# Performance work log

Hardware: AMD Instinct MI355X
Metric: run time of the kernel (lower is better)

The kernel has to match this reference:

```python
import jax, jax.numpy as jnp
import numpy as np

N_ATOMS = 100_000
N_PAIRS = 6_400_000
CUTOFF = 5.0
CUTON = 4.0


def setup_inputs() -> dict:
    key = jax.random.key(0)
    k = jax.random.split(key, 4)
    atomic_numbers = jax.random.uniform(k[0], (N_ATOMS,), jnp.float32, 1.0, 94.0)
    displacements = jax.random.normal(k[1], (N_PAIRS, 3), jnp.float32) * 2.0
    idx_i = jnp.sort(jax.random.randint(k[2], (N_PAIRS,), 0, N_ATOMS, jnp.int32))
    idx_j = jax.random.randint(k[3], (N_PAIRS,), 0, N_ATOMS, jnp.int32)
    atom_mask = jnp.ones((N_ATOMS,), jnp.float32)
    batch_segments = jnp.zeros((N_ATOMS,), jnp.int32)
    batch_mask = jnp.ones((N_PAIRS,), jnp.float32)
    # ZBL parameters (non-trainable constants from setup())
    a_coefficient = jnp.asarray(0.8854, jnp.float32)
    a_exponent = jnp.asarray(0.23, jnp.float32)
    phi_coefficients = jnp.array([0.18175, 0.50986, 0.28022, 0.02817], jnp.float32)
    phi_exponents = jnp.array([3.1998, 0.94229, 0.4029, 0.20162], jnp.float32)
    return dict(
        atomic_numbers=atomic_numbers,
        displacements=displacements,
        idx_i=idx_i,
        idx_j=idx_j,
        atom_mask=atom_mask,
        batch_segments=batch_segments,
        batch_mask=batch_mask,
        batch_size=1,
        a_coefficient=a_coefficient,
        a_exponent=a_exponent,
        phi_coefficients=phi_coefficients,
        phi_exponents=phi_exponents,
    )


def _switch_fn(distances):
    # smooth 1 -> 0 switch between CUTON and CUTOFF
    x = (CUTOFF - distances) / (CUTOFF - CUTON)
    poly = ((6.0 * x - 15.0) * x + 10.0) * x ** 3
    return jnp.where(distances < CUTON, 1.0, jnp.where(distances >= CUTOFF, 0.0, poly))


def reference(atomic_numbers, displacements, idx_i, idx_j, atom_mask,
              batch_segments, batch_mask, batch_size,
              a_coefficient, a_exponent, phi_coefficients, phi_exponents):
    distances = jnp.maximum(jnp.linalg.norm(displacements, axis=-1), 1e-10)  # [E]
    switch_off = _switch_fn(distances)

    za = jnp.power(atomic_numbers, jnp.abs(a_exponent))  # [N]
    denominator = jnp.maximum(za[idx_i] + za[idx_j], 1e-10)  # [E]
    a_ij = jnp.abs(a_coefficient) / denominator
    arguments = distances / a_ij  # [E]

    coefficients = jax.nn.softmax(jnp.abs(phi_coefficients))  # [4]
    exponents = jnp.abs(phi_exponents)  # [4]
    log_terms = -exponents[None, :] * arguments[:, None]  # [E,4]
    max_log = jnp.max(log_terms, axis=1, keepdims=True)
    # NOTE: faithful to the original -- max_log is never added back
    phi = jnp.sum(coefficients[None, :] * jnp.exp(log_terms - max_log), axis=1)  # [E]

    log_repulsion = (jnp.log(0.5)
                     + jnp.log(atomic_numbers[idx_i])
                     + jnp.log(atomic_numbers[idx_j])
                     - jnp.log(distances)
                     + jnp.log(jnp.maximum(phi, 1e-30))
                     + jnp.log(jnp.maximum(switch_off, 1e-30)))
    repulsion = jnp.exp(log_repulsion) * batch_mask  # [E]

    Erep = jax.ops.segment_sum(repulsion, segment_ids=idx_i,
                               num_segments=atomic_numbers.shape[0])  # [N]
    Erep = Erep * atom_mask
    return Erep[..., None, None, None]
```

## Files before the change

kernel.cpp:

```cpp
#include <hip/hip_runtime.h>
#include <math.h>


__global__ __launch_bounds__(256) void zbl_prep_kernel(
    const float* __restrict__ z, const float* __restrict__ a_coef,
    const float* __restrict__ a_exp, const float* __restrict__ phi_c,
    const float* __restrict__ phi_e, float2* __restrict__ tab,
    float* __restrict__ out, float* __restrict__ consts, int n_atoms) {
  int n = blockIdx.x * blockDim.x + threadIdx.x;
  if (n < n_atoms) {
    float zi = z[n];
    float ae = fabsf(a_exp[0]);
    tab[n] = make_float2(zi, powf(zi, ae));
    out[n] = 0.0f;
  }
  if (blockIdx.x == 0 && threadIdx.x == 0) {
    float c[4];
    float m = -1e30f;
    for (int k = 0; k < 4; ++k) { c[k] = fabsf(phi_c[k]); m = fmaxf(m, c[k]); }
    float s = 0.0f;
    for (int k = 0; k < 4; ++k) { c[k] = expf(c[k] - m); s += c[k]; }
    float inv_s = 1.0f / s;
    for (int k = 0; k < 4; ++k) consts[k] = c[k] * inv_s;
    for (int k = 0; k < 4; ++k) consts[4 + k] = fabsf(phi_e[k]);
    consts[8] = 1.0f / fabsf(a_coef[0]);
  }
}

__global__ __launch_bounds__(256) void zbl_edge_kernel(
    const float* __restrict__ disp, const int* __restrict__ idx_i,
    const int* __restrict__ idx_j, const float* __restrict__ bmask,
    const float2* __restrict__ tab, const float* __restrict__ consts,
    float* __restrict__ out, int n_edges) {
  int e = blockIdx.x * blockDim.x + threadIdx.x;
  int lane = threadIdx.x & 63;

  float v = 0.0f;
  int key = -1;
  if (e < n_edges) {
    int i = idx_i[e];
    int j = idx_j[e];
    float dx = disp[3 * e + 0];
    float dy = disp[3 * e + 1];
    float dz = disp[3 * e + 2];
    float d = sqrtf(dx * dx + dy * dy + dz * dz);
    d = fmaxf(d, 1e-10f);

    float x = 5.0f - d;
    float poly = ((6.0f * x - 15.0f) * x + 10.0f) * x * x * x;
    float sw = (d < 4.0f) ? 1.0f : ((d >= 5.0f) ? 0.0f : poly);

    float2 ti = tab[i];
    float2 tj = tab[j];
    float denom = fmaxf(ti.y + tj.y, 1e-10f);
    float arg = d * denom * consts[8];

    float e0 = consts[4], e1 = consts[5], e2 = consts[6], e3 = consts[7];
    float l0 = -e0 * arg, l1 = -e1 * arg, l2 = -e2 * arg, l3 = -e3 * arg;
    float m = fmaxf(fmaxf(l0, l1), fmaxf(l2, l3));
    float phi = consts[0] * expf(l0 - m) + consts[1] * expf(l1 - m) +
                consts[2] * expf(l2 - m) + consts[3] * expf(l3 - m);

    float rep = 0.5f * ti.x * tj.x / d * fmaxf(phi, 1e-30f) *
                fmaxf(sw, 1e-30f) * bmask[e];
    v = rep;
    key = i;
  }

  for (int off = 1; off < 64; off <<= 1) {
    float v2 = __shfl_down(v, off, 64);
    int k2 = __shfl_down(key, off, 64);
    if (lane + off < 64 && k2 == key) v += v2;
  }
  int kup = __shfl_up(key, 1, 64);
  if (key >= 0 && (lane == 0 || kup != key)) atomicAdd(&out[key], v);
}

__global__ __launch_bounds__(256) void zbl_mask_kernel(
    const float* __restrict__ mask, float* __restrict__ out, int n_atoms) {
  int n = blockIdx.x * blockDim.x + threadIdx.x;
  if (n < n_atoms) out[n] *= mask[n];
}

extern "C" void kernel_launch(void* const* d_in, const int* in_sizes, int n_in,
                              void* d_out, int out_size, void* d_ws,
                              size_t ws_size, hipStream_t stream) {
  const float* atomic_numbers = (const float*)d_in[0];
  const float* disp           = (const float*)d_in[1];
  const int*   idx_i          = (const int*)d_in[2];
  const int*   idx_j          = (const int*)d_in[3];
  const float* atom_mask      = (const float*)d_in[4];
  const float* bmask          = (const float*)d_in[6];
  const float* a_coef         = (const float*)d_in[8];
  const float* a_exp          = (const float*)d_in[9];
  const float* phi_c          = (const float*)d_in[10];
  const float* phi_e          = (const float*)d_in[11];

  int n_atoms = in_sizes[0];
  int n_edges = in_sizes[2];

  float* out = (float*)d_out;
  float2* tab = (float2*)d_ws;
  float* consts = (float*)((char*)d_ws + (size_t)n_atoms * sizeof(float2));

  int atom_blocks = (n_atoms + 255) / 256;
  int edge_blocks = (n_edges + 255) / 256;

  zbl_prep_kernel<<<atom_blocks, 256, 0, stream>>>(
      atomic_numbers, a_coef, a_exp, phi_c, phi_e, tab, out, consts, n_atoms);
  zbl_edge_kernel<<<edge_blocks, 256, 0, stream>>>(
      disp, idx_i, idx_j, bmask, tab, consts, out, n_edges);
  zbl_mask_kernel<<<atom_blocks, 256, 0, stream>>>(atom_mask, out, n_atoms);
}
```

Before: 52.82 us.

## Simplify ZBL phi algebraically, fold atom mask into atomics, unroll edges per wave

The max-subtracted softmax-style phi is rewritten so the smallest exponent term becomes a constant and the other three use exp2 of the exponent differences. This drops one exp and the max computation per edge. The coefficient division is folded into the precomputed constants, and rsq replaces sqrt plus divide. The separate mask kernel is removed by multiplying atom_mask inside each atomicAdd, and each wave now handles 256 edges in four unrolled chunks. Fast intrinsics may change rounding slightly, and the edge at the smallest exponent is assumed to always be the max.

Measured after the change: 53.58 us. No clear change (+1.4%).

```diff
diff --git a/kernel.cpp b/kernel.cpp
--- a/kernel.cpp
+++ b/kernel.cpp
@@ -1,5 +1,7 @@
 #include <hip/hip_runtime.h>
 #include <math.h>
+
+#define LOG2E 1.4426950408889634f
 
 
 __global__ __launch_bounds__(256) void zbl_prep_kernel(
@@ -11,19 +13,32 @@
   if (n < n_atoms) {
     float zi = z[n];
     float ae = fabsf(a_exp[0]);
-    tab[n] = make_float2(zi, powf(zi, ae));
+    float za = __builtin_amdgcn_exp2f(ae * __builtin_amdgcn_logf(zi));
+    tab[n] = make_float2(zi, za);
     out[n] = 0.0f;
   }
   if (blockIdx.x == 0 && threadIdx.x == 0) {
-    float c[4];
+    float c[4], e2[4];
     float m = -1e30f;
     for (int k = 0; k < 4; ++k) { c[k] = fabsf(phi_c[k]); m = fmaxf(m, c[k]); }
     float s = 0.0f;
     for (int k = 0; k < 4; ++k) { c[k] = expf(c[k] - m); s += c[k]; }
-    float inv_s = 1.0f / s;
-    for (int k = 0; k < 4; ++k) consts[k] = c[k] * inv_s;
-    for (int k = 0; k < 4; ++k) consts[4 + k] = fabsf(phi_e[k]);
-    consts[8] = 1.0f / fabsf(a_coef[0]);
+    for (int k = 0; k < 4; ++k) c[k] /= s;
+    int kmin = 0;
+    for (int k = 0; k < 4; ++k) {
+      e2[k] = fabsf(phi_e[k]) * LOG2E;
+      if (e2[k] < e2[kmin]) kmin = k;
+    }
+    float inv_a = 1.0f / fabsf(a_coef[0]);
+    consts[0] = c[kmin];
+    int p = 1;
+    for (int k = 0; k < 4; ++k) {
+      if (k != kmin) {
+        consts[p] = c[k];
+        consts[3 + p] = (e2[k] - e2[kmin]) * inv_a;
+        ++p;
+      }
+    }
   }
 }
 
@@ -31,55 +46,52 @@
     const float* __restrict__ disp, const int* __restrict__ idx_i,
     const int* __restrict__ idx_j, const float* __restrict__ bmask,
     const float2* __restrict__ tab, const float* __restrict__ consts,
-    float* __restrict__ out, int n_edges) {
-  int e = blockIdx.x * blockDim.x + threadIdx.x;
-  int lane = threadIdx.x & 63;
+    const float* __restrict__ amask, float* __restrict__ out, int n_edges) {
+  const int lane = threadIdx.x & 63;
+  const long wave = (long)blockIdx.x * (blockDim.x >> 6) + (threadIdx.x >> 6);
+  const long base = wave * 256;
 
-  float v = 0.0f;
-  int key = -1;
-  if (e < n_edges) {
-    int i = idx_i[e];
-    int j = idx_j[e];
-    float dx = disp[3 * e + 0];
-    float dy = disp[3 * e + 1];
-    float dz = disp[3 * e + 2];
-    float d = sqrtf(dx * dx + dy * dy + dz * dz);
-    d = fmaxf(d, 1e-10f);
+  const float c0 = consts[0], c1 = consts[1], c2 = consts[2], c3 = consts[3];
+  const float dd1 = consts[4], dd2 = consts[5], dd3 = consts[6];
 
-    float x = 5.0f - d;
-    float poly = ((6.0f * x - 15.0f) * x + 10.0f) * x * x * x;
-    float sw = (d < 4.0f) ? 1.0f : ((d >= 5.0f) ? 0.0f : poly);
+  #pragma unroll
+  for (int c = 0; c < 4; ++c) {
+    const long e = base + (long)(c << 6) + lane;
+    int key = -1;
+    float v = 0.0f;
+    if (e < (long)n_edges) {
+      const int i = idx_i[e];
+      const int j = idx_j[e];
+      const float dx = disp[3 * e + 0];
+      const float dy = disp[3 * e + 1];
+      const float dz = disp[3 * e + 2];
+      float n2 = fmaxf(dx * dx + dy * dy + dz * dz, 1e-20f);
+      float r = __builtin_amdgcn_rsqf(n2);
+      float d = n2 * r;
+      float x = 5.0f - d;
+      float poly = ((6.0f * x - 15.0f) * x + 10.0f) * x * x * x;
+      float sw = (d < 4.0f) ? 1.0f : ((d >= 5.0f) ? 0.0f : poly);
+      float2 ti = tab[i];
+      float2 tj = tab[j];
+      float q = d * fmaxf(ti.y + tj.y, 1e-10f);
+      float phi = c0 + c1 * __builtin_amdgcn_exp2f(-dd1 * q)
+                     + c2 * __builtin_amdgcn_exp2f(-dd2 * q)
+                     + c3 * __builtin_amdgcn_exp2f(-dd3 * q);
+      v = 0.5f * ti.x * tj.x * r * fmaxf(phi, 1e-30f) *
+          fmaxf(sw, 1e-30f) * bmask[e];
+      key = i;
+    }
 
-    float2 ti = tab[i];
-    float2 tj = tab[j];
-    float denom = fmaxf(ti.y + tj.y, 1e-10f);
-    float arg = d * denom * consts[8];
-
-    float e0 = consts[4], e1 = consts[5], e2 = consts[6], e3 = consts[7];
-    float l0 = -e0 * arg, l1 = -e1 * arg, l2 = -e2 * arg, l3 = -e3 * arg;
-    float m = fmaxf(fmaxf(l0, l1), fmaxf(l2, l3));
-    float phi = consts[0] * expf(l0 - m) + consts[1] * expf(l1 - m) +
-                consts[2] * expf(l2 - m) + consts[3] * expf(l3 - m);
-
-    float rep = 0.5f * ti.x * tj.x / d * fmaxf(phi, 1e-30f) *
-                fmaxf(sw, 1e-30f) * bmask[e];
-    v = rep;
-    key = i;
+    #pragma unroll
+    for (int off = 1; off < 64; off <<= 1) {
+      float v2 = __shfl_down(v, off, 64);
+      int k2 = __shfl_down(key, off, 64);
+      if (lane + off < 64 && k2 == key) v += v2;
+    }
+    int kup = __shfl_up(key, 1, 64);
+    if (key >= 0 && (lane == 0 || kup != key))
+      atomicAdd(&out[key], v * amask[key]);
   }
-
-  for (int off = 1; off < 64; off <<= 1) {
-    float v2 = __shfl_down(v, off, 64);
-    int k2 = __shfl_down(key, off, 64);
-    if (lane + off < 64 && k2 == key) v += v2;
-  }
-  int kup = __shfl_up(key, 1, 64);
-  if (key >= 0 && (lane == 0 || kup != key)) atomicAdd(&out[key], v);
-}
-
-__global__ __launch_bounds__(256) void zbl_mask_kernel(
-    const float* __restrict__ mask, float* __restrict__ out, int n_atoms) {
-  int n = blockIdx.x * blockDim.x + threadIdx.x;
-  if (n < n_atoms) out[n] *= mask[n];
 }
 
 extern "C" void kernel_launch(void* const* d_in, const int* in_sizes, int n_in,
@@ -104,11 +116,11 @@
   float* consts = (float*)((char*)d_ws + (size_t)n_atoms * sizeof(float2));
 
   int atom_blocks = (n_atoms + 255) / 256;
-  int edge_blocks = (n_edges + 255) / 256;
+  long waves = ((long)n_edges + 255) / 256;
+  int edge_blocks = (int)((waves + 3) / 4);
 
   zbl_prep_kernel<<<atom_blocks, 256, 0, stream>>>(
       atomic_numbers, a_coef, a_exp, phi_c, phi_e, tab, out, consts, n_atoms);
   zbl_edge_kernel<<<edge_blocks, 256, 0, stream>>>(
-      disp, idx_i, idx_j, bmask, tab, consts, out, n_edges);
-  zbl_mask_kernel<<<atom_blocks, 256, 0, stream>>>(atom_mask, out, n_atoms);
+      disp, idx_i, idx_j, bmask, tab, consts, atom_mask, out, n_edges);
 }
```
